# Optimization experiments

Hardware: AMD Instinct MI355X
Metric: run time of the kernel (lower is better)

The kernel has to match this reference:

```python
import jax, jax.numpy as jnp
import numpy as np

B, C, H, W = 2, 256, 128, 128
O = 256          # out_channels
KH = KW = 3
K = KH * KW      # 9 kernel taps
PAD, DIL = 1, 1


def setup_inputs() -> dict:
    key = jax.random.key(0)
    k1, k2, k3, k4, k5 = jax.random.split(key, 5)
    x = jax.random.normal(k1, (B, C, H, W), dtype=jnp.float32)
    # offset/mask predicting conv: 3*groups*K = 27 output channels.
    # scaled small so predicted offsets are O(1) pixels (torch inits these to 0).
    w_off = jax.random.normal(k2, (3 * K, C, KH, KW), dtype=jnp.float32) * 0.01
    b_off = jax.random.normal(k3, (3 * K,), dtype=jnp.float32) * 0.01
    # main weight is 1x1, later tiled to 3x3 (weight.repeat([1,1,3,3]))
    stdv = 1.0 / np.sqrt(C * KH * KW)
    weight = jax.random.uniform(k4, (O, C, 1, 1), dtype=jnp.float32, minval=-stdv, maxval=stdv)
    bias = jax.random.normal(k5, (O,), dtype=jnp.float32) * 0.01
    return {"x": x, "w_off": w_off, "b_off": b_off, "weight": weight, "bias": bias}


def _bilinear_gather(img, py, px):
    # img: [C,H,W]; py/px: [K,H,W] float sample coords. Zero outside bounds.
    y0 = jnp.floor(py).astype(jnp.int32)
    x0 = jnp.floor(px).astype(jnp.int32)
    ly = py - y0
    lx = px - x0

    def corner(yc, xc):
        valid = (yc >= 0) & (yc < H) & (xc >= 0) & (xc < W)
        v = img[:, jnp.clip(yc, 0, H - 1), jnp.clip(xc, 0, W - 1)]  # [C,K,H,W]
        return jnp.where(valid[None], v, 0.0)

    return (corner(y0, x0) * ((1 - ly) * (1 - lx))[None]
            + corner(y0, x0 + 1) * ((1 - ly) * lx)[None]
            + corner(y0 + 1, x0) * (ly * (1 - lx))[None]
            + corner(y0 + 1, x0 + 1) * (ly * lx)[None])


def reference(x, w_off, b_off, weight, bias):
    # --- offset/mask prediction conv (3x3, pad 1) ---
    tmp = jax.lax.conv_general_dilated(
        x, w_off, window_strides=(1, 1), padding=((PAD, PAD), (PAD, PAD)),
        rhs_dilation=(DIL, DIL), dimension_numbers=("NCHW", "OIHW", "NCHW"))
    tmp = tmp + b_off[None, :, None, None]
    o1, o2, mask = tmp[:, :K], tmp[:, K:2 * K], tmp[:, 2 * K:]
    offset = jnp.concatenate([o1, o2], axis=1)          # [B, 2K, H, W]
    dy = offset[:, 0::2]                                # [B, K, H, W]
    dx = offset[:, 1::2]
    # softmax over the SPATIAL axis per mask channel (as in the source)
    mask = jax.nn.softmax(mask.reshape(B, K, H * W), axis=2).reshape(B, K, H, W)

    # --- sampling grid ---
    kk = jnp.arange(K)
    ki = (kk // KW).astype(jnp.float32)
    kj = (kk % KW).astype(jnp.float32)
    base_y = ki[:, None, None] * DIL - PAD + jnp.arange(H, dtype=jnp.float32)[None, :, None]
    base_x = kj[:, None, None] * DIL - PAD + jnp.arange(W, dtype=jnp.float32)[None, None, :]
    py = dy + base_y[None]                              # [B, K, H, W]
    px = dx + base_x[None]

    sampled = jax.vmap(_bilinear_gather)(x, py, px)     # [B, C, K, H, W]
    sampled = sampled * mask[:, None]                   # modulated

    # weight.repeat([1,1,3,3]) -> same 1x1 weight at every tap
    Wk = jnp.tile(weight, (1, 1, KH, KW)).reshape(O, C, K)
    out = jnp.einsum("bckhw,ock->bohw", sampled, Wk) + bias[None, :, None, None]
    return out
```

## Files before the change

kernel.cpp:

```cpp
#include <hip/hip_runtime.h>
#include <hip/hip_fp16.h>

#define Bx 2
#define Cx 256
#define Hx 128
#define Wx 128
#define HWx (Hx*Wx)
#define Ox 256
#define Kx 9
#define NOFF 27
#define KK 2304

#define SLOT 80
#define NSLOT 102
#define ABUF (NSLOT*SLOT)

typedef __attribute__((ext_vector_type(8))) _Float16 f16x8;
typedef __attribute__((ext_vector_type(4))) float f32x4;


__device__ __forceinline__ unsigned short f2h(float f) {
    return __half_as_ushort(__float2half_rn(f));
}

__global__ __launch_bounds__(256) void k_pt(
        const float* __restrict__ x, const float* __restrict__ w_off,
        const float* __restrict__ weight,
        unsigned short* __restrict__ xtb, unsigned short* __restrict__ wbf,
        unsigned short* __restrict__ wq, float* __restrict__ stats) {
    if (blockIdx.x >= 2048) {
        if (blockIdx.x == 2048 && threadIdx.x < 32) stats[threadIdx.x] = 0.f;
        int i = (blockIdx.x - 2048) * 256 + threadIdx.x;
        if (i < 73728) {
            int e    = i & 7;
            int lane = (i >> 3) & 63;
            int frag = i >> 9;
            int t    = frag % 9;
            int sph  = frag / 9;
            int s    = sph & 1;
            int ph   = (sph >> 1) & 3;
            int wn   = sph >> 3;
            int col  = lane & 15, quad = lane >> 4;
            int oc   = wn * 16 + col;
            int c    = ph * 64 + s * 32 + quad * 8 + e;
            float v  = (oc < NOFF) ? w_off[(oc * Cx + c) * 9 + t] : 0.f;
            wbf[i] = f2h(v);
        } else {
            int j = i - 73728;
            wq[j] = f2h(weight[j]);
        }
        return;
    }
    __shared__ float tl[64][65];
    int tid = threadIdx.x;
    int t   = blockIdx.x;
    int b   = t >> 10;
    int r2  = t & 1023;
    int hw0 = (r2 >> 2) * 64;
    int c0  = (r2 & 3) * 64;
#pragma unroll
    for (int r = 0; r < 4; r++) {
        int cl = r * 16 + (tid >> 4);
        int hl = (tid & 15) * 4;
        const float4 v = *(const float4*)&x[((size_t)(b * Cx + c0 + cl)) * HWx + hw0 + hl];
        tl[cl][hl + 0] = v.x; tl[cl][hl + 1] = v.y; tl[cl][hl + 2] = v.z; tl[cl][hl + 3] = v.w;
    }
    __syncthreads();
#pragma unroll
    for (int r = 0; r < 4; r++) {
        int hl = r * 16 + (tid >> 4);
        int cl = (tid & 15) * 4;
        ushort4 o;
        o.x = f2h(tl[cl + 0][hl]); o.y = f2h(tl[cl + 1][hl]);
        o.z = f2h(tl[cl + 2][hl]); o.w = f2h(tl[cl + 3][hl]);
        *(ushort4*)&xtb[((size_t)b * HWx + hw0 + hl) * Cx + c0 + cl] = o;
    }
}

__global__ __launch_bounds__(256, 4) void k1_mfma(
        const unsigned short* __restrict__ xtb, const unsigned short* __restrict__ wbf,
        const float* __restrict__ b_off, float* __restrict__ tmp_t,
        float* __restrict__ stats) {
    int band = blockIdx.x & 7;
    int idx  = blockIdx.x >> 3;
    int y    = band * 16 + (idx >> 2);
    int qt   = idx & 3;
    int px0  = qt * 32;
    int b    = blockIdx.y;

    __shared__ unsigned short As[2 * ABUF];
    __shared__ float wsum[2][9];
    int tid  = threadIdx.x;
    int wave = tid >> 6, lane = tid & 63;
    int quad = lane >> 4, col = lane & 15;
    int wmh  = wave >> 1;
    int wn   = wave & 1;

    const unsigned short* xb = xtb + (size_t)b * HWx * Cx;
    const unsigned short* sp[4];
    int  sdst[4];
    bool sstp[4], sldp[4];
#pragma unroll
    for (int i = 0; i < 4; i++) {
        int u = tid + i * 256;
        bool uv = (u < 816);
        int slot = u >> 3;
        int ci   = (u & 7) * 8;
        int r = (slot >= 68) ? 2 : (slot >= 34 ? 1 : 0);
        int p = slot - r * 34;
        int yy = y + r - 1;
        int px = px0 + p - 1;
        bool ib = uv && (yy >= 0) && (yy < Hx) && (px >= 0) && (px < Wx);
        int lin = ib ? (yy * Wx + px) : 0;
        sp[i]   = xb + (size_t)lin * Cx + ci;
        sdst[i] = slot * SLOT + ci;
        sstp[i] = uv;
        sldp[i] = ib;
    }

    f32x4 acc = {};
    const unsigned short* wfb = wbf + ((size_t)(wn * 72 * 64 + lane)) * 8;
    int abase = (wmh * 16 + col) * SLOT + quad * 8;

    {
        uint4 sreg[4];
#pragma unroll
        for (int i = 0; i < 4; i++)
            sreg[i] = sldp[i] ? *(const uint4*)(sp[i]) : make_uint4(0u, 0u, 0u, 0u);
#pragma unroll
        for (int i = 0; i < 4; i++)
            if (sstp[i]) *(uint4*)&As[sdst[i]] = sreg[i];
    }
    __syncthreads();

#pragma unroll 1
    for (int ph = 0; ph < 4; ph++) {
        const unsigned short* Ab = As + (ph & 1) * ABUF;
        unsigned short*       Aw = As + ((ph & 1) ^ 1) * ABUF;
        uint4 sreg[4];
        if (ph < 3) {
#pragma unroll
            for (int i = 0; i < 4; i++)
                sreg[i] = sldp[i] ? *(const uint4*)(sp[i] + (ph + 1) * 64)
                                  : make_uint4(0u, 0u, 0u, 0u);
        }
#pragma unroll
        for (int s = 0; s < 2; s++) {
            int fbase = (ph * 2 + s) * 9;
            f16x8 breg[9];
#pragma unroll
            for (int t = 0; t < 9; t++)
                breg[t] = *(const f16x8*)(wfb + ((size_t)(fbase + t) << 9));
#pragma unroll
            for (int r = 0; r < 3; r++)
#pragma unroll
            for (int dc = 0; dc < 3; dc++) {
                f16x8 a0 = *(const f16x8*)&Ab[(r * 34 + dc) * SLOT + abase + s * 32];
                acc = __builtin_amdgcn_mfma_f32_16x16x32_f16(a0, breg[r * 3 + dc], acc, 0, 0, 0);
            }
        }
        if (ph < 3) {
#pragma unroll
            for (int i = 0; i < 4; i++)
                if (sstp[i]) *(uint4*)&Aw[sdst[i]] = sreg[i];
        }
        __syncthreads();
    }

    float* orow = tmp_t + ((size_t)(b * HWx) + (size_t)y * Wx + px0) * 32;
    int oc = wn * 16 + col;
    float bo = (oc < NOFF) ? b_off[oc] : 0.f;
#pragma unroll
    for (int r4 = 0; r4 < 4; r4++) {
        int pxd = wmh * 16 + quad * 4 + r4;
        float v = acc[r4] + bo;
        acc[r4] = v;
        orow[(size_t)pxd * 32 + oc] = v;
    }

    float s4 = __expf(acc[0]) + __expf(acc[1]) + __expf(acc[2]) + __expf(acc[3]);
    s4 += __shfl_xor(s4, 16);
    s4 += __shfl_xor(s4, 32);
    if (wn == 1 && quad == 0 && col >= 2 && col <= 10)
        wsum[wmh][col - 2] = s4;
    __syncthreads();
    if (tid < 9)
        atomicAdd(&stats[b * 9 + tid], wsum[0][tid] + wsum[1][tid]);
}

__global__ __launch_bounds__(256) void k35_fused(
        const unsigned short* __restrict__ xtb, const float* __restrict__ tmp_t,
        const float* __restrict__ stats, const unsigned short* __restrict__ wq,
        const float* __restrict__ bias, float* __restrict__ out) {
    __shared__ __half2 lwh[64][36];
    __shared__ int     lo[64][36];
    __shared__ unsigned short As[64][264];
    __shared__ float sst9[9];
    int tid  = threadIdx.x;
    int band = blockIdx.x & 7;
    int sub  = blockIdx.x >> 3;
    int b    = blockIdx.y;
    int px0  = (band * 32 + sub) * 64;

    if (tid < 9) sst9[tid] = 256.f / stats[b * Kx + tid];
    __syncthreads();

    for (int u = tid; u < 576; u += 256) {
        int px = u / 9, k = u - px * 9;
        int hw = px0 + px;
        int y  = hw >> 7;
        int xx = hw & (Wx - 1);
        const float* trow = tmp_t + ((size_t)b * HWx + hw) * 32;
        float dy = trow[2 * k];
        float dx = trow[2 * k + 1];
        float lg = trow[18 + k];
        float m  = __expf(lg) * sst9[k];
        float py = dy + (float)(k / 3 - 1 + y);
        float px_ = dx + (float)(k % 3 - 1 + xx);
        float fy = floorf(py), fx = floorf(px_);
        int y0 = (int)fy, x0 = (int)fx;
        float ly = py - fy, lx = px_ - fx;
        float w00 = (1.f - ly) * (1.f - lx) * m;
        float w01 = (1.f - ly) * lx * m;
        float w10 = ly * (1.f - lx) * m;
        float w11 = ly * lx * m;
        int y1 = y0 + 1, x1 = x0 + 1;
        bool vy0 = (y0 >= 0) & (y0 < Hx), vy1 = (y1 >= 0) & (y1 < Hx);
        bool vx0 = (x0 >= 0) & (x0 < Wx), vx1 = (x1 >= 0) & (x1 < Wx);
        int cy0 = min(max(y0, 0), Hx - 1), cy1 = min(max(y1, 0), Hx - 1);
        int cx0 = min(max(x0, 0), Wx - 1), cx1 = min(max(x1, 0), Wx - 1);
        float a00 = (vy0 && vx0) ? w00 : 0.f;
        float a01 = (vy0 && vx1) ? w01 : 0.f;
        float a10 = (vy1 && vx0) ? w10 : 0.f;
        float a11 = (vy1 && vx1) ? w11 : 0.f;
        lwh[px][4 * k + 0] = __half2half2(__float2half_rn(a00));  lo[px][4 * k + 0] = cy0 * Wx + cx0;
        lwh[px][4 * k + 1] = __half2half2(__float2half_rn(a01));  lo[px][4 * k + 1] = cy0 * Wx + cx1;
        lwh[px][4 * k + 2] = __half2half2(__float2half_rn(a10));  lo[px][4 * k + 2] = cy1 * Wx + cx0;
        lwh[px][4 * k + 3] = __half2half2(__float2half_rn(a11));  lo[px][4 * k + 3] = cy1 * Wx + cx1;
    }
    __syncthreads();

    int wave = tid >> 6;
    int lane = tid & 63;
    int half = lane >> 5;
    int li   = lane & 31;
    const unsigned short* xb = xtb + (size_t)b * HWx * Cx + li * 8;
    const __half2 uns = __half2half2(__float2half_rn(1.f / 256.f));
#pragma unroll 1
    for (int pass = 0; pass < 8; pass++) {
        int px = pass * 8 + wave * 2 + half;
        __half2 a0 = __half2half2(__ushort_as_half(0));
        __half2 a1 = a0, a2 = a0, a3 = a0;
#pragma unroll
        for (int j = 0; j < 36; j++) {
            __half2 w = lwh[px][j];
            int   off = lo[px][j];
            uint4 v = *(const uint4*)(xb + (size_t)off * Cx);
            a0 = __hfma2(w, *(__half2*)&v.x, a0);
            a1 = __hfma2(w, *(__half2*)&v.y, a1);
            a2 = __hfma2(w, *(__half2*)&v.z, a2);
            a3 = __hfma2(w, *(__half2*)&v.w, a3);
        }
        a0 = __hmul2(a0, uns); a1 = __hmul2(a1, uns);
        a2 = __hmul2(a2, uns); a3 = __hmul2(a3, uns);
        uint4 r;
        r.x = *(unsigned*)&a0; r.y = *(unsigned*)&a1;
        r.z = *(unsigned*)&a2; r.w = *(unsigned*)&a3;
        *(uint4*)&As[px][li * 8] = r;
    }
    __syncthreads();

    int quad = lane >> 4, col = lane & 15;
    f32x4 acc[4][4] = {};
#pragma unroll
    for (int ki = 0; ki < 8; ki++) {
        int k0 = ki * 32;
        f16x8 a[4], w[4];
#pragma unroll
        for (int mt = 0; mt < 4; mt++)
            a[mt] = *(const f16x8*)&As[mt * 16 + col][k0 + quad * 8];
#pragma unroll
        for (int nt = 0; nt < 4; nt++)
            w[nt] = *(const f16x8*)(wq + (size_t)(wave * 64 + nt * 16 + col) * Cx + k0 + quad * 8);
#pragma unroll
        for (int mt = 0; mt < 4; mt++)
#pragma unroll
            for (int nt = 0; nt < 4; nt++)
                acc[mt][nt] = __builtin_amdgcn_mfma_f32_16x16x32_f16(a[mt], w[nt], acc[mt][nt], 0, 0, 0);
    }

#pragma unroll
    for (int nt = 0; nt < 4; nt++) {
        int oc = wave * 64 + nt * 16 + col;
        float bo = bias[oc];
#pragma unroll
        for (int mt = 0; mt < 4; mt++) {
            int hw = px0 + mt * 16 + quad * 4;
            float4 v;
            v.x = acc[mt][nt][0] + bo; v.y = acc[mt][nt][1] + bo;
            v.z = acc[mt][nt][2] + bo; v.w = acc[mt][nt][3] + bo;
            *(float4*)&out[((size_t)(b * Ox + oc)) * HWx + hw] = v;
        }
    }
}

extern "C" void kernel_launch(void* const* d_in, const int* in_sizes, int n_in,
                              void* d_out, int out_size, void* d_ws, size_t ws_size,
                              hipStream_t stream) {
    const float*    x      = (const float*)d_in[0];
    const float*    w_off  = (const float*)d_in[1];
    const float*    b_off  = (const float*)d_in[2];
    const float*    weight = (const float*)d_in[3];
    const float*    bias   = (const float*)d_in[4];
    float* out = (float*)d_out;
    float* ws  = (float*)d_ws;

    float*          tmp_t = ws;
    unsigned short* wbf   = (unsigned short*)(ws + 1048640);
    unsigned short* xtb   = (unsigned short*)(ws + 1085504);
    unsigned short* wq    = (unsigned short*)(ws + 5279808);
    float*          stats = ws + 5312576;

    k_pt<<<dim3(2592), 256, 0, stream>>>(x, w_off, weight, xtb, wbf, wq, stats);
    k1_mfma<<<dim3(512, Bx), 256, 0, stream>>>(xtb, wbf, b_off, tmp_t, stats);
    k35_fused<<<dim3(256, Bx), 256, 0, stream>>>(xtb, tmp_t, stats, wq, bias, out);
}
```

Measured before the change: 146.1 us.

## Stage neighborhood window of x in LDS per channel chunk for bilinear gather

The fused gather+GEMM kernel now loads a 7x72 pixel window of the channel-last fp16 input into shared memory, one 32-channel chunk at a time, and serves bilinear corner reads from LDS. Samples that fall outside the window fall back to global loads. The gather and the MFMA GEMM are interleaved per channel chunk, so the full 64x256 A tile no longer has to sit in LDS. The intent is to cut redundant global/L2 traffic from the overlapping 36 corner reads per pixel. The cost is extra syncthreads per chunk, a divergent branch on the fallback path, and swizzled window staging.

```diff
diff --git a/kernel.cpp b/kernel.cpp
--- a/kernel.cpp
+++ b/kernel.cpp
@@ -14,6 +14,10 @@
 #define SLOT 80
 #define NSLOT 102
 #define ABUF (NSLOT*SLOT)
+
+#define WROWS 7
+#define WCOLS 72
+#define WCELLS (WROWS*WCOLS)
 
 typedef __attribute__((ext_vector_type(8))) _Float16 f16x8;
 typedef __attribute__((ext_vector_type(4))) float f32x4;
@@ -192,15 +196,17 @@
         const unsigned short* __restrict__ xtb, const float* __restrict__ tmp_t,
         const float* __restrict__ stats, const unsigned short* __restrict__ wq,
         const float* __restrict__ bias, float* __restrict__ out) {
-    __shared__ __half2 lwh[64][36];
-    __shared__ int     lo[64][36];
-    __shared__ unsigned short As[64][264];
+    __shared__ int2 lop[64][37];
+    __shared__ unsigned short win[WCELLS * 32];
+    __shared__ unsigned short Asc[64 * 40];
     __shared__ float sst9[9];
     int tid  = threadIdx.x;
     int band = blockIdx.x & 7;
     int sub  = blockIdx.x >> 3;
     int b    = blockIdx.y;
     int px0  = (band * 32 + sub) * 64;
+    int y    = px0 >> 7;
+    int x0   = px0 & (Wx - 1);
 
     if (tid < 9) sst9[tid] = 256.f / stats[b * Kx + tid];
     __syncthreads();
@@ -208,54 +214,97 @@
     for (int u = tid; u < 576; u += 256) {
         int px = u / 9, k = u - px * 9;
         int hw = px0 + px;
-        int y  = hw >> 7;
+        int yy = hw >> 7;
         int xx = hw & (Wx - 1);
         const float* trow = tmp_t + ((size_t)b * HWx + hw) * 32;
         float dy = trow[2 * k];
         float dx = trow[2 * k + 1];
         float lg = trow[18 + k];
         float m  = __expf(lg) * sst9[k];
-        float py = dy + (float)(k / 3 - 1 + y);
+        float py = dy + (float)(k / 3 - 1 + yy);
         float px_ = dx + (float)(k % 3 - 1 + xx);
         float fy = floorf(py), fx = floorf(px_);
-        int y0 = (int)fy, x0 = (int)fx;
+        int y0 = (int)fy, x0c = (int)fx;
         float ly = py - fy, lx = px_ - fx;
         float w00 = (1.f - ly) * (1.f - lx) * m;
         float w01 = (1.f - ly) * lx * m;
         float w10 = ly * (1.f - lx) * m;
         float w11 = ly * lx * m;
-        int y1 = y0 + 1, x1 = x0 + 1;
+        int y1 = y0 + 1, x1 = x0c + 1;
         bool vy0 = (y0 >= 0) & (y0 < Hx), vy1 = (y1 >= 0) & (y1 < Hx);
-        bool vx0 = (x0 >= 0) & (x0 < Wx), vx1 = (x1 >= 0) & (x1 < Wx);
+        bool vx0 = (x0c >= 0) & (x0c < Wx), vx1 = (x1 >= 0) & (x1 < Wx);
         int cy0 = min(max(y0, 0), Hx - 1), cy1 = min(max(y1, 0), Hx - 1);
-        int cx0 = min(max(x0, 0), Wx - 1), cx1 = min(max(x1, 0), Wx - 1);
+        int cx0 = min(max(x0c, 0), Wx - 1), cx1 = min(max(x1, 0), Wx - 1);
         float a00 = (vy0 && vx0) ? w00 : 0.f;
         float a01 = (vy0 && vx1) ? w01 : 0.f;
         float a10 = (vy1 && vx0) ? w10 : 0.f;
         float a11 = (vy1 && vx1) ? w11 : 0.f;
-        lwh[px][4 * k + 0] = __half2half2(__float2half_rn(a00));  lo[px][4 * k + 0] = cy0 * Wx + cx0;
-        lwh[px][4 * k + 1] = __half2half2(__float2half_rn(a01));  lo[px][4 * k + 1] = cy0 * Wx + cx1;
-        lwh[px][4 * k + 2] = __half2half2(__float2half_rn(a10));  lo[px][4 * k + 2] = cy1 * Wx + cx0;
-        lwh[px][4 * k + 3] = __half2half2(__float2half_rn(a11));  lo[px][4 * k + 3] = cy1 * Wx + cx1;
-    }
-    __syncthreads();
-
-    int wave = tid >> 6;
-    int lane = tid & 63;
-    int half = lane >> 5;
-    int li   = lane & 31;
-    const unsigned short* xb = xtb + (size_t)b * HWx * Cx + li * 8;
+#pragma unroll
+        for (int c = 0; c < 4; c++) {
+            int cy = (c < 2) ? cy0 : cy1;
+            int cx = (c & 1) ? cx1 : cx0;
+            float aw = (c == 0) ? a00 : (c == 1) ? a01 : (c == 2) ? a10 : a11;
+            int rr = cy - (y - 3);
+            int rc = cx - (x0 - 4);
+            int cell = (rr >= 0 && rr < WROWS && rc >= 0 && rc < WCOLS)
+                     ? (rr * WCOLS + rc) : 511;
+            __half2 wh = __half2half2(__float2half_rn(aw));
+            int2 pk;
+            pk.x = *(int*)&wh;
+            pk.y = ((cy * Wx + cx) << 9) | cell;
+            lop[px][4 * k + c] = pk;
+        }
+    }
+
+    const unsigned short* xb = xtb + (size_t)b * HWx * Cx;
+    const unsigned short* wsp[8];
+    int wdst[8];
+#pragma unroll
+    for (int i = 0; i < 8; i++) {
+        int u = tid + i * 256;
+        if (u < WCELLS * 4) {
+            int cell = u >> 2, qs = u & 3;
+            int wr = cell / WCOLS, wc = cell - wr * WCOLS;
+            int row = min(max(y - 3 + wr, 0), Hx - 1);
+            int cg  = min(max(x0 - 4 + wc, 0), Wx - 1);
+            wsp[i]  = xb + ((size_t)(row * Wx + cg)) * Cx + qs * 8;
+            wdst[i] = cell * 32 + (qs ^ ((cell >> 1) & 3)) * 8;
+        } else {
+            wsp[i]  = xb;
+            wdst[i] = -1;
+        }
+    }
+
+    int wave = tid >> 6, lane = tid & 63;
+    int g    = lane >> 2;
+    int q    = lane & 3;
+    int mypx = wave * 16 + g;
+    int quad = lane >> 4, col = lane & 15;
     const __half2 uns = __half2half2(__float2half_rn(1.f / 256.f));
+    f32x4 acc[4][4] = {};
+
+    __syncthreads();
+#pragma unroll
+    for (int i = 0; i < 8; i++)
+        if (wdst[i] >= 0) *(uint4*)&win[wdst[i]] = *(const uint4*)(wsp[i]);
+    __syncthreads();
+
 #pragma unroll 1
-    for (int pass = 0; pass < 8; pass++) {
-        int px = pass * 8 + wave * 2 + half;
+    for (int p = 0; p < 8; p++) {
         __half2 a0 = __half2half2(__ushort_as_half(0));
         __half2 a1 = a0, a2 = a0, a3 = a0;
 #pragma unroll
         for (int j = 0; j < 36; j++) {
-            __half2 w = lwh[px][j];
-            int   off = lo[px][j];
-            uint4 v = *(const uint4*)(xb + (size_t)off * Cx);
+            int2 t = lop[mypx][j];
+            __half2 w = *(__half2*)&t.x;
+            int cell = t.y & 511;
+            uint4 v;
+            if (cell != 511) {
+                int sl = q ^ ((cell >> 1) & 3);
+                v = *(const uint4*)&win[cell * 32 + sl * 8];
+            } else {
+                v = *(const uint4*)(xb + ((size_t)(t.y >> 9)) * Cx + p * 32 + q * 8);
+            }
             a0 = __hfma2(w, *(__half2*)&v.x, a0);
             a1 = __hfma2(w, *(__half2*)&v.y, a1);
             a2 = __hfma2(w, *(__half2*)&v.z, a2);
@@ -266,27 +315,28 @@
         uint4 r;
         r.x = *(unsigned*)&a0; r.y = *(unsigned*)&a1;
         r.z = *(unsigned*)&a2; r.w = *(unsigned*)&a3;
-        *(uint4*)&As[px][li * 8] = r;
-    }
-    __syncthreads();
-
-    int quad = lane >> 4, col = lane & 15;
-    f32x4 acc[4][4] = {};
-#pragma unroll
-    for (int ki = 0; ki < 8; ki++) {
-        int k0 = ki * 32;
-        f16x8 a[4], w[4];
+        *(uint4*)&Asc[mypx * 40 + q * 8] = r;
+        __syncthreads();
+
+        if (p < 7) {
+#pragma unroll
+            for (int i = 0; i < 8; i++)
+                if (wdst[i] >= 0)
+                    *(uint4*)&win[wdst[i]] = *(const uint4*)(wsp[i] + (p + 1) * 32);
+        }
+        f16x8 av[4], wv[4];
+#pragma unroll
+        for (int nt = 0; nt < 4; nt++)
+            wv[nt] = *(const f16x8*)(wq + (size_t)(wave * 64 + nt * 16 + col) * Cx + p * 32 + quad * 8);
 #pragma unroll
         for (int mt = 0; mt < 4; mt++)
-            a[mt] = *(const f16x8*)&As[mt * 16 + col][k0 + quad * 8];
-#pragma unroll
-        for (int nt = 0; nt < 4; nt++)
-            w[nt] = *(const f16x8*)(wq + (size_t)(wave * 64 + nt * 16 + col) * Cx + k0 + quad * 8);
+            av[mt] = *(const f16x8*)&Asc[(mt * 16 + col) * 40 + quad * 8];
 #pragma unroll
         for (int mt = 0; mt < 4; mt++)
 #pragma unroll
             for (int nt = 0; nt < 4; nt++)
-                acc[mt][nt] = __builtin_amdgcn_mfma_f32_16x16x32_f16(a[mt], w[nt], acc[mt][nt], 0, 0, 0);
+                acc[mt][nt] = __builtin_amdgcn_mfma_f32_16x16x32_f16(av[mt], wv[nt], acc[mt][nt], 0, 0, 0);
+        __syncthreads();
     }
 
 #pragma unroll
```

Measured after the change: 197.2 us. +34.9%, slower.
